# Optimization experiments

Hardware: AMD Instinct MI355X
Metric: run time of the kernel (lower is better)

Reference implementation:

```python
import jax, jax.numpy as jnp
import numpy as np

N = 100000      # nodes
E = 3200000     # edges
H = 64          # node_hidden_dim
DIN = 15        # node_input_dim
DOUT = 12       # output_dim
NT = 5          # num_edge_type
G = 256         # graphs in batch
STEPS = 6       # num_step_prop


def setup_inputs() -> dict:
    key = jax.random.key(0)
    ks = jax.random.split(key, 24)
    s = 0.1
    n = lambda k, shp: jax.random.normal(k, shp, jnp.float32) * s
    return {
        "x": jax.random.normal(ks[0], (N, DIN), jnp.float32),
        "edge_index": jax.random.randint(ks[1], (2, E), 0, N, dtype=jnp.int32),
        "edge_attr": jax.random.randint(ks[2], (E,), 0, NT, dtype=jnp.int32),
        "batch": jnp.sort(jax.random.randint(ks[3], (N,), 0, G, dtype=jnp.int32)),
        "lin0_w": n(ks[4], (DIN, H)), "lin0_b": n(ks[5], (H,)),
        "edge_embed": n(ks[6], (NT, H * H)),
        "conv_bias": n(ks[7], (H,)),
        "gru_w_ih": n(ks[8], (H, 3 * H)), "gru_w_hh": n(ks[9], (H, 3 * H)),
        "gru_b_ih": n(ks[10], (3 * H,)), "gru_b_hh": n(ks[11], (3 * H,)),
        "i_w1": n(ks[12], (2 * H, H)), "i_b1": n(ks[13], (H,)),
        "i_w2": n(ks[14], (H, DOUT)), "i_b2": n(ks[15], (DOUT,)),
        "j_w1": n(ks[16], (H, H)), "j_b1": n(ks[17], (H,)),
        "j_w2": n(ks[18], (H, DOUT)), "j_b2": n(ks[19], (DOUT,)),
    }


def reference(x, edge_index, edge_attr, batch,
              lin0_w, lin0_b, edge_embed, conv_bias,
              gru_w_ih, gru_w_hh, gru_b_ih, gru_b_hh,
              i_w1, i_b1, i_w2, i_b2, j_w1, j_b1, j_w2, j_b2):
    src, dst = edge_index[0], edge_index[1]
    W_types = edge_embed.reshape(NT, H, H)  # per edge-type [H_in, H_out]

    # in-degree for mean aggregation (PyG: isolated nodes get 0)
    deg = jax.ops.segment_sum(jnp.ones((E,), x.dtype), dst, num_segments=N)
    deg = jnp.maximum(deg, 1.0)[:, None]

    out0 = jax.nn.relu(x @ lin0_w + lin0_b)
    out = out0
    h = out0

    for _ in range(STEPS):
        # NNConv: per-edge matmul m_e = x_src[e] @ W[type_e].
        # Only NT=5 edge types exist -> precompute all 5 transforms, then gather.
        T = jnp.einsum('nh,tho->nto', out, W_types)        # [N, NT, H]
        msg = T[src, edge_attr]                            # [E, H] gather
        agg = jax.ops.segment_sum(msg, dst, num_segments=N) / deg + conv_bias
        m = jax.nn.relu(agg)

        # GRU cell (torch gate order: r, z, n)
        gx = m @ gru_w_ih + gru_b_ih
        gh = h @ gru_w_hh + gru_b_hh
        xr, xz, xn = jnp.split(gx, 3, axis=1)
        hr, hz, hn = jnp.split(gh, 3, axis=1)
        r = jax.nn.sigmoid(xr + hr)
        z = jax.nn.sigmoid(xz + hz)
        nn_ = jnp.tanh(xn + r * hn)
        h = (1.0 - z) * nn_ + z * h
        out = h

    # gated readout
    i = jax.nn.sigmoid(
        jax.nn.sigmoid(jnp.concatenate([out, out0], axis=1) @ i_w1 + i_b1) @ i_w2 + i_b2)
    j = jax.nn.sigmoid(out @ j_w1 + j_b1) @ j_w2 + j_b2
    gated = i * j                                          # [N, DOUT]
    return jax.ops.segment_sum(gated, batch, num_segments=G)  # [G, DOUT]
```

## Files before the change

kernel.cpp:

```cpp
#include <hip/hip_runtime.h>
#include <hip/hip_bf16.h>

typedef __hip_bfloat16 bf16;
using short8 = __attribute__((ext_vector_type(8))) short;
using f32x4  = __attribute__((ext_vector_type(4))) float;
using f32x2  = __attribute__((ext_vector_type(2))) float;

#define MFMA16(a,b,c) __builtin_amdgcn_mfma_f32_16x16x32_bf16((a),(b),(c),0,0,0)
#define MAXBUCK 4096
#define SB 72
#define MSTR 72
#define SRCCAP 1024
#define CHK 8192
#define BCAP 2816

__device__ __forceinline__ float b2f(bf16 v){ return __bfloat162float(v); }
__device__ __forceinline__ bf16  f2b(float v){ return __float2bfloat16(v); }
__device__ __forceinline__ float sigmf(float x){ return 1.f/(1.f+__expf(-x)); }
__device__ __forceinline__ float tanhfast(float x){
  x = fminf(fmaxf(x,-15.f),15.f);
  float e = __expf(2.f*x);
  return (e-1.f)/(e+1.f);
}
__device__ __forceinline__ short8 ld_frag(const bf16* p){
  return *reinterpret_cast<const short8*>(p);
}
__device__ __forceinline__ short f2bits(float f){
  unsigned u = __builtin_bit_cast(unsigned, f);
  unsigned r = (u + 0x7FFFu + ((u>>16)&1u)) >> 16;
  return (short)r;
}
__device__ __forceinline__ f32x2 pk_add(f32x2 a, f32x2 b){
  f32x2 d;
  asm("v_pk_add_f32 %0, %1, %2" : "=v"(d) : "v"(a), "v"(b));
  return d;
}
__device__ __forceinline__ unsigned cvtpk_bf16(float lo, float hi){
  unsigned r;
  asm("v_cvt_pk_bf16_f32 %0, %1, %2" : "=v"(r) : "v"(lo), "v"(hi));
  return r;
}

__device__ __forceinline__ f32x2 cvt8lo(unsigned w){
  f32x2 r;
  asm("v_cvt_pk_f32_fp8 %0, %1" : "=v"(r) : "v"(w));
  return r;
}
__device__ __forceinline__ f32x2 cvt8hi(unsigned w){
  return cvt8lo(w >> 16);
}
__device__ __forceinline__ unsigned short f32pair_to_fp8(float a, float b){
  unsigned r = 0;
  asm("v_cvt_pk_fp8_f32 %0, %1, %2" : "+v"(r) : "v"(a), "v"(b));
  return (unsigned short)(r & 0xffffu);
}


__global__ void k_sniff(const unsigned int* __restrict__ x, int* __restrict__ flag){
  int t = threadIdx.x;
  int good = 0;
  for (int i=t; i<4096; i+=256){
    unsigned w = x[i];
    unsigned e = (w>>23)&0xFFu;
    unsigned m = w & 0x7FFFFFFFu;
    if ((e>=100u && e<=150u) || m==0u) good++;
  }
  __shared__ int sm[256];
  sm[t]=good; __syncthreads();
  if (t==0){ int s=0; for (int k=0;k<256;k++) s+=sm[k]; *flag = (s>2048)?1:0; }
}

struct PtrPack { const void* p[17]; };

#define CAN_X     0
#define CAN_L0W   1500032
#define CAN_L0B   1500992
#define CAN_EE    1501056
#define CAN_CB    1521536
#define CAN_WIH   1521600
#define CAN_WHH   1533888
#define CAN_BIH   1546176
#define CAN_BHH   1546368
#define CAN_IW1   1546560
#define CAN_IB1   1554752
#define CAN_IW2   1554816
#define CAN_IB2   1555584
#define CAN_JW1   1555648
#define CAN_JB1   1559744
#define CAN_JW2   1559808
#define CAN_JB2   1560576
#define CAN_TOT   1560640

__global__ void k_canon(PtrPack pk, const int* __restrict__ flag, bf16* __restrict__ dst){
  static const int offs[17] = {CAN_X,CAN_L0W,CAN_L0B,CAN_EE,CAN_CB,CAN_WIH,CAN_WHH,
    CAN_BIH,CAN_BHH,CAN_IW1,CAN_IB1,CAN_IW2,CAN_IB2,CAN_JW1,CAN_JB1,CAN_JW2,CAN_JB2};
  static const int szs[17]  = {1500000,960,64,20480,64,12288,12288,192,192,8192,64,768,12,4096,64,768,12};
  int t = blockIdx.x*256+threadIdx.x;
  if (t >= CAN_TOT) return;
  int s = 0;
  #pragma unroll
  for (int k=1;k<17;k++) if (t >= offs[k]) s = k;
  int i = t - offs[s];
  float v = 0.f;
  if (i < szs[s]){
    if (*flag) v = ((const float*)pk.p[s])[i];
    else       v = b2f(((const bf16*)pk.p[s])[i]);
  }
  dst[t] = f2b(v);
}


__global__ __launch_bounds__(1024) void k_scan(const int* __restrict__ cnt, int n,
      int* __restrict__ ptr, int* __restrict__ cursor){
  __shared__ int ws[17];
  int tid = threadIdx.x, lane = tid&63, w = tid>>6;
  int run = 0;
  for (int base=0; base<n; base+=1024){
    int i = base + tid;
    int v = (i<n)? cnt[i] : 0;
    int incl = v;
    #pragma unroll
    for (int off=1; off<64; off<<=1){
      int t = __shfl_up(incl, off, 64);
      if (lane>=off) incl += t;
    }
    if (lane==63) ws[w] = incl;
    __syncthreads();
    if (tid==0){ int r=0; for (int k=0;k<16;k++){ int t=ws[k]; ws[k]=r; r+=t; } ws[16]=r; }
    __syncthreads();
    int excl = run + ws[w] + incl - v;
    if (i<n){
      ptr[i] = excl;
      if (cursor) cursor[i] = excl;
    }
    run += ws[16];
    __syncthreads();
  }
  if (tid==0) ptr[n] = run;
}

__global__ __launch_bounds__(512) void k_csort(const int* __restrict__ srcv,
      const int* __restrict__ dstv, const int* __restrict__ eav, int E_, int nb, int NC,
      unsigned int* __restrict__ bucketed, int* __restrict__ rs, int* __restrict__ bkt_cnt){
  __shared__ int lh[MAXBUCK];
  __shared__ int lofs[MAXBUCK];
  __shared__ int ws[9];
  int c = blockIdx.x, tid = threadIdx.x;
  int base = c*CHK, end = min(base+CHK, E_);
  for (int i=tid;i<nb;i+=512) lh[i]=0;
  __syncthreads();
  for (int i=base+tid; i<end; i+=512) atomicAdd(&lh[dstv[i]>>5], 1);
  __syncthreads();
  int lane=tid&63, w=tid>>6;
  int run=0;
  for (int bb=0; bb<nb; bb+=512){
    int i=bb+tid;
    int v=(i<nb)? lh[i]:0;
    int incl=v;
    #pragma unroll
    for (int off=1;off<64;off<<=1){
      int t=__shfl_up(incl,off,64);
      if (lane>=off) incl+=t;
    }
    if (lane==63) ws[w]=incl;
    __syncthreads();
    if (tid==0){ int r=0; for(int k=0;k<8;k++){int t=ws[k];ws[k]=r;r+=t;} ws[8]=r; }
    __syncthreads();
    if (i<nb) lofs[i]= run + ws[w] + incl - v;
    run += ws[8];
    __syncthreads();
  }
  for (int i=tid;i<nb;i+=512){
    rs[(size_t)i*NC + c] = base + lofs[i];
    int cntv = lh[i];
    if (cntv) atomicAdd(&bkt_cnt[i], cntv);
  }
  if (tid==0) rs[(size_t)nb*NC + c] = end;
  __syncthreads();
  for (int i=base+tid;i<end;i+=512){
    int d = dstv[i];
    int bin = d>>5;
    int pos = base + atomicAdd(&lofs[bin], 1);
    bucketed[pos] = (((unsigned)((d&31)*5 + eav[i]))<<17) | (unsigned)srcv[i];
  }
}

__global__ __launch_bounds__(256) void k_bsort2(const unsigned int* __restrict__ bucketed,
      const int* __restrict__ rs, int NC,
      const int* __restrict__ bkt_ptr, int nb, int E_,
      int* __restrict__ kptr, int* __restrict__ sorted_src,
      unsigned char* __restrict__ kperm){
  __shared__ unsigned sbuf[BCAP];
  __shared__ int rofs[1025];
  __shared__ int cnt[160], sc[160], cur[160];
  int b = blockIdx.x, tid = threadIdx.x;
  int s = bkt_ptr[b], e = bkt_ptr[b+1];
  int size = e - s;
  const int* rowA = rs + (size_t)b*NC;
  const int* rowB = rs + (size_t)(b+1)*NC;
  for (int c2=tid; c2<NC; c2+=256) rofs[c2] = rowB[c2] - rowA[c2];
  __syncthreads();
  if (tid==0){
    int acc=0;
    for (int c2=0;c2<NC;c2++){ int t=rofs[c2]; rofs[c2]=acc; acc+=t; }
    rofs[NC]=acc;
  }
  __syncthreads();
  bool staged = (size <= BCAP);
  if (staged){
    for (int c2=tid; c2<NC; c2+=256){
      int st = rowA[c2];
      int ln = rowB[c2] - st;
      int d0 = rofs[c2];
      for (int k=0;k<ln;k++) sbuf[d0+k] = bucketed[st+k];
    }
  }
  __syncthreads();
  if (tid<160) cnt[tid]=0;
  __syncthreads();
  if (staged){
    for (int i=tid;i<size;i+=256) atomicAdd(&cnt[sbuf[i]>>17], 1);
  } else {
    for (int c2=0;c2<NC;c2++){
      int st=rowA[c2], ln=rowB[c2]-st;
      for (int k=tid;k<ln;k+=256) atomicAdd(&cnt[bucketed[st+k]>>17], 1);
    }
  }
  __syncthreads();
  if (tid<160) sc[tid]=cnt[tid];
  __syncthreads();
  #pragma unroll
  for (int off=1; off<160; off<<=1){
    int v = 0;
    if (tid<160 && tid>=off) v = sc[tid-off];
    __syncthreads();
    if (tid<160) sc[tid] += v;
    __syncthreads();
  }
  if (tid<160){
    int basek = s + sc[tid] - cnt[tid];
    kptr[b*160+tid] = basek;
    cur[tid] = basek;
  }
  if (b==nb-1 && tid==0) kptr[(size_t)nb*160] = e;
  if (tid<160){
    int hbase = (tid<80)? 0 : 80;
    int me = cnt[tid];
    int r = 0;
    for (int j=0;j<80;j++){
      int jj = hbase+j;
      int cj = cnt[jj];
      r += (cj>me) || (cj==me && jj<tid);
    }
    kperm[((size_t)b*2 + (tid<80?0:1))*80 + r] = (unsigned char)(tid - hbase);
  }
  __syncthreads();
  if (staged){
    for (int i=tid;i<size;i+=256){
      unsigned p = sbuf[i];
      int pos = atomicAdd(&cur[p>>17], 1);
      sorted_src[pos] = (int)(p & 0x1FFFFu);
    }
  } else {
    for (int c2=0;c2<NC;c2++){
      int st=rowA[c2], ln=rowB[c2]-st;
      for (int k=tid;k<ln;k+=256){
        unsigned p = bucketed[st+k];
        int pos = atomicAdd(&cur[p>>17], 1);
        sorted_src[pos] = (int)(p & 0x1FFFFu);
      }
    }
  }
}

__global__ __launch_bounds__(256) void k_lin0(const bf16* __restrict__ x,
      const bf16* __restrict__ w, const bf16* __restrict__ b,
      bf16* __restrict__ out0, bf16* __restrict__ h,
      unsigned char* __restrict__ hq, int N_){
  int idx = blockIdx.x*256+threadIdx.x;
  int n = idx>>6, o = idx&63;
  if (n>=N_) return;
  float acc = b2f(b[o]);
  #pragma unroll
  for (int k=0;k<15;k++) acc += b2f(x[n*15+k]) * b2f(w[k*64+o]);
  float hv = fmaxf(acc,0.f);
  bf16 v = f2b(hv);
  out0[idx]=v; h[idx]=v;
  float hvn = __shfl_xor(hv, 1);
  if (!(o&1)) *(unsigned short*)(hq + (size_t)n*64 + o) = f32pair_to_fp8(hv, hvn);
}

__device__ __forceinline__ void d_swz(const unsigned short* src, int KS, int NC,
                                      unsigned short* dst, int nfrag, int t){
  if (t >= nfrag*64) return;
  int lane=t&63, frag=t>>6, cb=frag/KS, ks=frag%KS;
  int c = cb*16 + (lane&15);
  #pragma unroll
  for (int j=0;j<8;j++){
    int k = ks*32 + ((lane>>4)<<3) + j;
    dst[t*8+j] = (c<NC)? src[k*NC+c] : (unsigned short)0;
  }
}

__global__ __launch_bounds__(256) void k_prep(const bf16* __restrict__ ee,
      const bf16* __restrict__ wih, const bf16* __restrict__ whh,
      const bf16* __restrict__ iw1, const bf16* __restrict__ jw1,
      const bf16* __restrict__ iw2, const bf16* __restrict__ jw2,
      unsigned short* __restrict__ wall, unsigned short* __restrict__ wgru,
      unsigned short* __restrict__ wr1, unsigned short* __restrict__ wiw2s,
      unsigned short* __restrict__ wjw2s,
      const int* __restrict__ batch, int N_, int G_, int* __restrict__ gptr){
  int blk = blockIdx.x, tid = threadIdx.x;
  if (blk < 10){
    int t = blk*256+tid;
    if (t<2560){
      int lane=t&63, frag=t>>6, ct=frag/10, ks=frag%10;
      int c = ct*16 + (lane&15);
      #pragma unroll
      for (int j=0;j<8;j++){
        int k = ks*32 + ((lane>>4)<<3) + j;
        int tt = k>>6, kc = k&63;
        wall[t*8+j] = ((const unsigned short*)ee)[tt*4096 + kc*64 + c];
      }
    }
  } else if (blk < 16){
    d_swz((const unsigned short*)wih, 2, 192, wgru, 24, (blk-10)*256+tid);
  } else if (blk < 22){
    d_swz((const unsigned short*)whh, 2, 192, wgru+12288, 24, (blk-16)*256+tid);
  } else if (blk < 26){
    d_swz((const unsigned short*)iw1, 4, 64, wr1, 16, (blk-22)*256+tid);
  } else if (blk < 28){
    d_swz((const unsigned short*)jw1, 2, 64, wr1+8192, 8, (blk-26)*256+tid);
  } else if (blk == 28){
    d_swz((const unsigned short*)iw2, 2, 12, wiw2s, 2, tid);
  } else if (blk == 29){
    d_swz((const unsigned short*)jw2, 2, 12, wjw2s, 2, tid);
  } else {
    int g = (blk-30)*256+tid;
    if (g <= G_){
      int lo=0, hi=N_;
      while (lo<hi){ int mid=(lo+hi)>>1; if (batch[mid] < g) lo=mid+1; else hi=mid; }
      gptr[g]=lo;
    }
  }
}

__global__ __launch_bounds__(256,8) void k_step(const bf16* __restrict__ hin,
      bf16* __restrict__ hout,
      const unsigned char* __restrict__ hqin, unsigned char* __restrict__ hqout,
      const int* __restrict__ sorted_src, const int* __restrict__ kptr,
      const unsigned char* __restrict__ kperm,
      const unsigned short* __restrict__ wall, const unsigned short* __restrict__ wgru,
      const bf16* __restrict__ conv_bias, const bf16* __restrict__ bih,
      const bf16* __restrict__ bhh, int N_){
  __shared__ unsigned short Sb[80*SB];
  __shared__ int kp[81];
  __shared__ unsigned char pm[80];
  __shared__ char ubuf[SRCCAP*4 + 32];
  int* srcL = (int*)ubuf;
  unsigned short* m_s = (unsigned short*)ubuf;
  int tid=threadIdx.x, lane=tid&63, w=tid>>6;
  int b=blockIdx.x;
  if (tid<81) kp[tid]=kptr[(size_t)b*80+tid];
  if (tid<80) pm[tid]=kperm[(size_t)b*80+tid];
  __syncthreads();
  int s0g = kp[0];
  int elen = kp[80]-s0g;
  int cap = (elen<=SRCCAP)? elen : 0;
  for (int i=tid;i<cap;i+=256) srcL[i]=sorted_src[s0g+i]<<6;
  __syncthreads();
  int g=lane>>3, c=lane&7;
  const unsigned char* hp8 = hqin + (c<<3);
  const int sent = N_<<6;

  auto run_phase1 = [&](auto GET){
    #pragma unroll 1
    for (int jo=0;jo<5;jo++){
      int pbase = jo*16 + w*4;
      int p  = pm[pbase + (g&3)];
      int p0 = pm[pbase];
      int st = kp[p]-s0g, len = kp[p+1]-kp[p];
      int maxLen = kp[p0+1]-kp[p0];
      int sub = g>>2;
      f32x2 a01={0.f,0.f}, a23={0.f,0.f}, a45={0.f,0.f}, a67={0.f,0.f};
      for (int base=0; base<maxLen; base+=8){
        uint2 hv[4];
        #pragma unroll
        for (int u=0;u<4;u++){
          int idx = base + sub*4 + u;
          int s = GET(st+idx);
          s = (idx < len)? s : sent;
          hv[u] = *(const uint2*)(hp8 + (size_t)s);
        }
        #pragma unroll
        for (int u=0;u<4;u++){
          a01 = pk_add(a01, cvt8lo(hv[u].x));
          a23 = pk_add(a23, cvt8hi(hv[u].x));
          a45 = pk_add(a45, cvt8lo(hv[u].y));
          a67 = pk_add(a67, cvt8hi(hv[u].y));
        }
      }
      float a[8] = {a01.x,a01.y,a23.x,a23.y,a45.x,a45.y,a67.x,a67.y};
      #pragma unroll
      for (int j=0;j<8;j++) a[j] += __shfl_xor(a[j], 32);
      if (g<4){
        uint4 v;
        v.x = cvtpk_bf16(a[0],a[1]);
        v.y = cvtpk_bf16(a[2],a[3]);
        v.z = cvtpk_bf16(a[4],a[5]);
        v.w = cvtpk_bf16(a[6],a[7]);
        *reinterpret_cast<uint4*>(&Sb[(size_t)p*SB + c*8]) = v;
      }
    }
  };
  if (cap) run_phase1([&](int rel){ return srcL[rel]; });
  else     run_phase1([&](int rel){ return sorted_src[s0g+rel]<<6; });
  __syncthreads();

  int q=lane>>4, mr=lane&15;
  {
    int ct = w;
    f32x4 acc={0.f,0.f,0.f,0.f};
    #pragma unroll
    for (int ks=0;ks<10;ks++){
      int k0 = ks*32 + q*8;
      int tt = k0>>6, ch = k0&63;
      short8 af = *reinterpret_cast<const short8*>(&Sb[(size_t)(mr*5+tt)*SB + ch]);
      short8 bfrag = *(const short8*)(wall + (size_t)((ct*10+ks)*64+lane)*8);
      acc = MFMA16(af, bfrag, acc);
    }
    int col = ct*16+mr;
    float bi = b2f(conv_bias[col]);
    #pragma unroll
    for (int r=0;r<4;r++){
      int nl = q*4+r;
      int deg = kp[nl*5+5]-kp[nl*5];
      float dv = 1.f/fmaxf((float)deg,1.f);
      m_s[nl*MSTR+col] = (unsigned short)f2bits(fmaxf(acc[r]*dv+bi,0.f));
    }
  }
  __syncthreads();

  {
    int cc = w;
    int na = b*16+mr; if (na>N_-1) na=N_-1;
    short8 am0 = *(const short8*)(&m_s[mr*MSTR + q*8]);
    short8 am1 = *(const short8*)(&m_s[mr*MSTR + 32 + q*8]);
    short8 ah0 = ld_frag(hin + (size_t)na*64 + q*8);
    short8 ah1 = ld_frag(hin + (size_t)na*64 + 32 + q*8);
    const short8* Bw = reinterpret_cast<const short8*>(wgru);
    f32x4 xr={0.f,0.f,0.f,0.f}, xz=xr, xn=xr, hr=xr, hz=xr, hn=xr;
    xr = MFMA16(am0, Bw[((cc  )*2+0)*64+lane], xr);
    xr = MFMA16(am1, Bw[((cc  )*2+1)*64+lane], xr);
    xz = MFMA16(am0, Bw[((cc+4)*2+0)*64+lane], xz);
    xz = MFMA16(am1, Bw[((cc+4)*2+1)*64+lane], xz);
    xn = MFMA16(am0, Bw[((cc+8)*2+0)*64+lane], xn);
    xn = MFMA16(am1, Bw[((cc+8)*2+1)*64+lane], xn);
    hr = MFMA16(ah0, Bw[(24+(cc  )*2+0)*64+lane], hr);
    hr = MFMA16(ah1, Bw[(24+(cc  )*2+1)*64+lane], hr);
    hz = MFMA16(ah0, Bw[(24+(cc+4)*2+0)*64+lane], hz);
    hz = MFMA16(ah1, Bw[(24+(cc+4)*2+1)*64+lane], hz);
    hn = MFMA16(ah0, Bw[(24+(cc+8)*2+0)*64+lane], hn);
    hn = MFMA16(ah1, Bw[(24+(cc+8)*2+1)*64+lane], hn);
    int col = cc*16+mr;
    float bxr=b2f(bih[col]), bxz=b2f(bih[col+64]), bxn=b2f(bih[col+128]);
    float bhr=b2f(bhh[col]), bhz=b2f(bhh[col+64]), bhn=b2f(bhh[col+128]);
    #pragma unroll
    for (int r=0;r<4;r++){
      int row = q*4+r;
      int n = b*16+row;
      int nc = (n<N_)? n : N_-1;
      float rg = sigmf(xr[r]+bxr + hr[r]+bhr);
      float zg = sigmf(xz[r]+bxz + hz[r]+bhz);
      float ng = tanhfast(xn[r]+bxn + rg*(hn[r]+bhn));
      float ho = b2f(hin[(size_t)nc*64+col]);
      float hv = (1.f-zg)*ng + zg*ho;
      float hvn = __shfl_xor(hv, 1);
      if (n < N_){
        hout[(size_t)n*64+col] = f2b(hv);
        if (!(mr&1))
          *(unsigned short*)(hqout + (size_t)n*64 + col) = f32pair_to_fp8(hv, hvn);
      }
    }
  }
}

__global__ __launch_bounds__(256) void k_read(const bf16* __restrict__ h, const bf16* __restrict__ out0,
      const unsigned short* __restrict__ W, const bf16* __restrict__ ib1, const bf16* __restrict__ jb1,
      const unsigned short* __restrict__ iw2swz, const unsigned short* __restrict__ jw2swz,
      const bf16* __restrict__ ib2, const bf16* __restrict__ jb2,
      float* __restrict__ gated, int N_){
  __shared__ unsigned short lds[12288];
  __shared__ unsigned short sbuf[64*72];
  __shared__ unsigned short tbuf[64*72];
  { const int* s=(const int*)W; int* d=(int*)lds;
    for (int i=threadIdx.x;i<6144;i+=256) d[i]=s[i]; }
  __syncthreads();
  int tid=threadIdx.x, lane=tid&63, w=tid>>6, q=lane>>4;
  int nb = blockIdx.x*64 + w*16;
  int ar = nb + (lane&15); if (ar>N_-1) ar=N_-1;
  short8 ah0 = ld_frag(h + (size_t)ar*64 + q*8),    ah1 = ld_frag(h + (size_t)ar*64 + 32 + q*8);
  short8 ao0 = ld_frag(out0 + (size_t)ar*64 + q*8), ao1 = ld_frag(out0 + (size_t)ar*64 + 32 + q*8);
  const short8* Bi = reinterpret_cast<const short8*>(lds);
  const short8* Bj = reinterpret_cast<const short8*>(lds + 8192);
  int colb = lane&15;
  for (int cb=0; cb<4; cb++){
    f32x4 ai = {0.f,0.f,0.f,0.f};
    ai = MFMA16(ah0, Bi[(cb*4+0)*64+lane], ai);
    ai = MFMA16(ah1, Bi[(cb*4+1)*64+lane], ai);
    ai = MFMA16(ao0, Bi[(cb*4+2)*64+lane], ai);
    ai = MFMA16(ao1, Bi[(cb*4+3)*64+lane], ai);
    f32x4 aj = {0.f,0.f,0.f,0.f};
    aj = MFMA16(ah0, Bj[(cb*2+0)*64+lane], aj);
    aj = MFMA16(ah1, Bj[(cb*2+1)*64+lane], aj);
    int col = cb*16 + colb;
    float bi=b2f(ib1[col]), bj=b2f(jb1[col]);
    #pragma unroll
    for (int r=0;r<4;r++){
      int lrow = w*16 + q*4 + r;
      sbuf[lrow*72+col] = (unsigned short)f2bits(sigmf(ai[r]+bi));
      tbuf[lrow*72+col] = (unsigned short)f2bits(sigmf(aj[r]+bj));
    }
  }
  __syncthreads();
  int mr = lane&15;
  short8 as0 = *(const short8*)(&sbuf[(w*16+mr)*72 + q*8]);
  short8 as1 = *(const short8*)(&sbuf[(w*16+mr)*72 + 32 + q*8]);
  short8 at0 = *(const short8*)(&tbuf[(w*16+mr)*72 + q*8]);
  short8 at1 = *(const short8*)(&tbuf[(w*16+mr)*72 + 32 + q*8]);
  const short8* Bi2 = reinterpret_cast<const short8*>(iw2swz);
  const short8* Bj2 = reinterpret_cast<const short8*>(jw2swz);
  f32x4 ai = {0.f,0.f,0.f,0.f};
  ai = MFMA16(as0, Bi2[lane], ai);
  ai = MFMA16(as1, Bi2[64+lane], ai);
  f32x4 aj = {0.f,0.f,0.f,0.f};
  aj = MFMA16(at0, Bj2[lane], aj);
  aj = MFMA16(at1, Bj2[64+lane], aj);
  int col = lane&15;
  if (col<12){
    float bi=b2f(ib2[col]), bj=b2f(jb2[col]);
    #pragma unroll
    for (int r=0;r<4;r++){
      int row = nb + q*4 + r;
      if (row < N_) gated[(size_t)row*12+col] = sigmf(ai[r]+bi)*(aj[r]+bj);
    }
  }
}

__global__ __launch_bounds__(256) void k_graphsum(const float* __restrict__ gated,
      const int* __restrict__ gptr, const int* __restrict__ flag, void* __restrict__ outp){
  int g = blockIdx.x;
  int s = gptr[g], e = gptr[g+1];
  int tid = threadIdx.x;
  int c = tid & 15, rg = tid >> 4;
  float acc = 0.f;
  if (c < 12)
    for (int row = s + rg; row < e; row += 16) acc += gated[(size_t)row*12 + c];
  __shared__ float sm[256];
  sm[tid] = acc;
  __syncthreads();
  if (rg == 0 && c < 12){
    float t = 0.f;
    for (int k=0;k<16;k++) t += sm[k*16 + c];
    if (*flag) ((float*)outp)[g*12 + c] = t;
    else       ((bf16*) outp)[g*12 + c] = f2b(t);
  }
}


extern "C" void kernel_launch(void* const* d_in, const int* in_sizes, int n_in,
                              void* d_out, int out_size, void* d_ws, size_t ws_size,
                              hipStream_t stream){
  const int*  ei    = (const int*) d_in[1];
  const int*  ea    = (const int*) d_in[2];
  const int*  batch = (const int*) d_in[3];

  const int N_ = in_sizes[3];
  const int E_ = in_sizes[2];
  const int G_ = out_size / 12;
  const int nb  = (N_ + 31) >> 5;
  const int nbs = (N_ + 15) >> 4;
  const int NC  = (E_ + CHK - 1) / CHK;

  char* ws = (char*)d_ws;
  size_t off = 0;
  auto alloc = [&](size_t bytes)->size_t{
    size_t o = off; off += (bytes + 255) & ~(size_t)255; return o;
  };

  size_t oOut0   = alloc((size_t)N_*64*2);
  size_t oH0     = alloc((size_t)(N_+1)*64*2);
  size_t oH1     = alloc((size_t)(N_+1)*64*2);
  size_t oHq0    = alloc((size_t)(N_+1)*64);
  size_t oHq1    = alloc((size_t)(N_+1)*64);
  size_t oGated  = alloc((size_t)N_*12*4);
  size_t oBEdges = alloc((size_t)E_*4);
  size_t oSorted = alloc((size_t)E_*4 + 256);
  size_t oRS     = alloc((size_t)(nb+1)*NC*4);
  size_t oKptr   = alloc(((size_t)nb*160+2)*4);
  size_t oKperm  = alloc((size_t)nb*160);
  size_t oCanon  = alloc((size_t)CAN_TOT*2);
  size_t oCnt    = alloc((size_t)nb*4);
  size_t oBPtr   = alloc((size_t)(nb+1)*4);
  size_t oGptr   = alloc((size_t)(G_+1)*4);
  size_t oFlag   = alloc(256);
  size_t oWall   = alloc((size_t)20480*2);
  size_t oWgru   = alloc((size_t)24576*2);
  size_t oWr1    = alloc((size_t)12288*2);
  size_t oWiw2   = alloc((size_t)1024*2);
  size_t oWjw2   = alloc((size_t)1024*2);

  bf16*  out0    = (bf16*)(ws + oOut0);
  bf16*  h0      = (bf16*)(ws + oH0);
  bf16*  h1      = (bf16*)(ws + oH1);
  unsigned char* hq0 = (unsigned char*)(ws + oHq0);
  unsigned char* hq1 = (unsigned char*)(ws + oHq1);
  float* gated   = (float*)(ws + oGated);
  unsigned int* bucketed = (unsigned int*)(ws + oBEdges);
  int*   sorted_src = (int*)(ws + oSorted);
  int*   rs      = (int*)(ws + oRS);
  int*   kptr    = (int*)(ws + oKptr);
  unsigned char* kperm = (unsigned char*)(ws + oKperm);
  bf16*  can     = (bf16*)(ws + oCanon);
  int*   bkt_cnt = (int*)(ws + oCnt);
  int*   bkt_ptr = (int*)(ws + oBPtr);
  int*   gptr    = (int*)(ws + oGptr);
  int*   flag    = (int*)(ws + oFlag);
  unsigned short* wall  = (unsigned short*)(ws + oWall);
  unsigned short* wgru  = (unsigned short*)(ws + oWgru);
  unsigned short* wr1   = (unsigned short*)(ws + oWr1);
  unsigned short* wiw2s = (unsigned short*)(ws + oWiw2);
  unsigned short* wjw2s = (unsigned short*)(ws + oWjw2);

  const bf16* xC    = can + CAN_X;
  const bf16* l0wC  = can + CAN_L0W;
  const bf16* l0bC  = can + CAN_L0B;
  const bf16* eeC   = can + CAN_EE;
  const bf16* cbC   = can + CAN_CB;
  const bf16* wihC  = can + CAN_WIH;
  const bf16* whhC  = can + CAN_WHH;
  const bf16* bihC  = can + CAN_BIH;
  const bf16* bhhC  = can + CAN_BHH;
  const bf16* iw1C  = can + CAN_IW1;
  const bf16* ib1C  = can + CAN_IB1;
  const bf16* iw2C  = can + CAN_IW2;
  const bf16* ib2C  = can + CAN_IB2;
  const bf16* jw1C  = can + CAN_JW1;
  const bf16* jb1C  = can + CAN_JB1;
  const bf16* jw2C  = can + CAN_JW2;
  const bf16* jb2C  = can + CAN_JB2;

  PtrPack pk;
  pk.p[0]=d_in[0];  pk.p[1]=d_in[4];  pk.p[2]=d_in[5];  pk.p[3]=d_in[6];
  pk.p[4]=d_in[7];  pk.p[5]=d_in[8];  pk.p[6]=d_in[9];  pk.p[7]=d_in[10];
  pk.p[8]=d_in[11]; pk.p[9]=d_in[12]; pk.p[10]=d_in[13]; pk.p[11]=d_in[14];
  pk.p[12]=d_in[15]; pk.p[13]=d_in[16]; pk.p[14]=d_in[17]; pk.p[15]=d_in[18];
  pk.p[16]=d_in[19];

  const int gNw  = (N_+63)/64;

  k_sniff<<<1, 256, 0, stream>>>((const unsigned int*)d_in[0], flag);
  k_canon<<<(CAN_TOT+255)/256, 256, 0, stream>>>(pk, flag, can);
  hipMemsetAsync(ws + oCnt, 0, (size_t)nb*4, stream);
  hipMemsetAsync(ws + oH0 + (size_t)N_*128, 0, 128, stream);
  hipMemsetAsync(ws + oH1 + (size_t)N_*128, 0, 128, stream);
  hipMemsetAsync(ws + oHq0 + (size_t)N_*64, 0, 64, stream);
  hipMemsetAsync(ws + oHq1 + (size_t)N_*64, 0, 64, stream);
  k_csort<<<NC, 512, 0, stream>>>(ei, ei + E_, ea, E_, nb, NC, bucketed, rs, bkt_cnt);
  k_scan<<<1, 1024, 0, stream>>>(bkt_cnt, nb, bkt_ptr, nullptr);
  k_bsort2<<<nb, 256, 0, stream>>>(bucketed, rs, NC, bkt_ptr, nb, E_, kptr, sorted_src, kperm);
  k_lin0<<<(N_*64+255)/256, 256, 0, stream>>>(xC, l0wC, l0bC, out0, h0, hq0, N_);
  k_prep<<<32, 256, 0, stream>>>(eeC, wihC, whhC, iw1C, jw1C, iw2C, jw2C,
                                 wall, wgru, wr1, wiw2s, wjw2s, batch, N_, G_, gptr);

  bf16* hb[2] = {h0, h1};
  unsigned char* hqb[2] = {hq0, hq1};
  for (int step = 0; step < 6; ++step){
    k_step<<<nbs, 256, 0, stream>>>(hb[step&1], hb[(step+1)&1],
                                    hqb[step&1], hqb[(step+1)&1],
                                    sorted_src, kptr, kperm,
                                    wall, wgru, cbC, bihC, bhhC, N_);
  }
  bf16* hfin = hb[0];

  k_read<<<gNw, 256, 0, stream>>>(hfin, out0, wr1, ib1C, jb1C, wiw2s, wjw2s,
                                  ib2C, jb2C, gated, N_);
  k_graphsum<<<G_, 256, 0, stream>>>(gated, gptr, flag, d_out);
}
```

Baseline: 669.0 us.

## Fold memsets into sniff kernel, enlarge sort chunks, parallelize bucket staging

```diff
diff --git a/kernel.cpp b/kernel.cpp
--- a/kernel.cpp
+++ b/kernel.cpp
@@ -11,7 +11,8 @@
 #define SB 72
 #define MSTR 72
 #define SRCCAP 1024
-#define CHK 8192
+#define CHK 32768
+#define MAXNC 128
 #define BCAP 2816
 
 __device__ __forceinline__ float b2f(bf16 v){ return __bfloat162float(v); }
@@ -55,9 +56,20 @@
   return (unsigned short)(r & 0xffffu);
 }
 
-
-__global__ void k_sniff(const unsigned int* __restrict__ x, int* __restrict__ flag){
+__global__ void k_sniff(const unsigned int* __restrict__ x, int* __restrict__ flag,
+      int* __restrict__ bkt_cnt, int nb,
+      int* __restrict__ s0, int* __restrict__ s1,
+      int* __restrict__ s2, int* __restrict__ s3){
   int t = threadIdx.x;
+  if (blockIdx.x == 1){
+    for (int i=t;i<nb;i+=256) bkt_cnt[i]=0;
+    return;
+  }
+  if (blockIdx.x == 2){
+    if (t<32){ s0[t]=0; s1[t]=0; }
+    if (t<16){ s2[t]=0; s3[t]=0; }
+    return;
+  }
   int good = 0;
   for (int i=t; i<4096; i+=256){
     unsigned w = x[i];
@@ -139,21 +151,21 @@
   if (tid==0) ptr[n] = run;
 }
 
-__global__ __launch_bounds__(512) void k_csort(const int* __restrict__ srcv,
+__global__ __launch_bounds__(1024) void k_csort(const int* __restrict__ srcv,
       const int* __restrict__ dstv, const int* __restrict__ eav, int E_, int nb, int NC,
       unsigned int* __restrict__ bucketed, int* __restrict__ rs, int* __restrict__ bkt_cnt){
   __shared__ int lh[MAXBUCK];
   __shared__ int lofs[MAXBUCK];
-  __shared__ int ws[9];
+  __shared__ int ws[17];
   int c = blockIdx.x, tid = threadIdx.x;
   int base = c*CHK, end = min(base+CHK, E_);
-  for (int i=tid;i<nb;i+=512) lh[i]=0;
-  __syncthreads();
-  for (int i=base+tid; i<end; i+=512) atomicAdd(&lh[dstv[i]>>5], 1);
+  for (int i=tid;i<nb;i+=1024) lh[i]=0;
+  __syncthreads();
+  for (int i=base+tid; i<end; i+=1024) atomicAdd(&lh[dstv[i]>>5], 1);
   __syncthreads();
   int lane=tid&63, w=tid>>6;
   int run=0;
-  for (int bb=0; bb<nb; bb+=512){
+  for (int bb=0; bb<nb; bb+=1024){
     int i=bb+tid;
     int v=(i<nb)? lh[i]:0;
     int incl=v;
@@ -164,20 +176,20 @@
     }
     if (lane==63) ws[w]=incl;
     __syncthreads();
-    if (tid==0){ int r=0; for(int k=0;k<8;k++){int t=ws[k];ws[k]=r;r+=t;} ws[8]=r; }
+    if (tid==0){ int r=0; for(int k=0;k<16;k++){int t=ws[k];ws[k]=r;r+=t;} ws[16]=r; }
     __syncthreads();
     if (i<nb) lofs[i]= run + ws[w] + incl - v;
-    run += ws[8];
-    __syncthreads();
-  }
-  for (int i=tid;i<nb;i+=512){
+    run += ws[16];
+    __syncthreads();
+  }
+  for (int i=tid;i<nb;i+=1024){
     rs[(size_t)i*NC + c] = base + lofs[i];
     int cntv = lh[i];
     if (cntv) atomicAdd(&bkt_cnt[i], cntv);
   }
   if (tid==0) rs[(size_t)nb*NC + c] = end;
   __syncthreads();
-  for (int i=base+tid;i<end;i+=512){
+  for (int i=base+tid;i<end;i+=1024){
     int d = dstv[i];
     int bin = d>>5;
     int pos = base + atomicAdd(&lofs[bin], 1);
@@ -191,28 +203,46 @@
       int* __restrict__ kptr, int* __restrict__ sorted_src,
       unsigned char* __restrict__ kperm){
   __shared__ unsigned sbuf[BCAP];
-  __shared__ int rofs[1025];
+  __shared__ int rofs[MAXNC+1];
+  __shared__ int rstart[MAXNC];
+  __shared__ int scan2[2][MAXNC];
   __shared__ int cnt[160], sc[160], cur[160];
   int b = blockIdx.x, tid = threadIdx.x;
   int s = bkt_ptr[b], e = bkt_ptr[b+1];
   int size = e - s;
   const int* rowA = rs + (size_t)b*NC;
   const int* rowB = rs + (size_t)(b+1)*NC;
-  for (int c2=tid; c2<NC; c2+=256) rofs[c2] = rowB[c2] - rowA[c2];
-  __syncthreads();
-  if (tid==0){
-    int acc=0;
-    for (int c2=0;c2<NC;c2++){ int t=rofs[c2]; rofs[c2]=acc; acc+=t; }
-    rofs[NC]=acc;
-  }
-  __syncthreads();
-  bool staged = (size <= BCAP);
+  bool fits = (NC <= MAXNC);
+  if (fits){
+    int v = 0;
+    if (tid < NC){
+      int a = rowA[tid];
+      rstart[tid] = a;
+      v = rowB[tid] - a;
+    }
+    if (tid < MAXNC) scan2[0][tid] = v;
+    __syncthreads();
+    int pp = 0;
+    #pragma unroll
+    for (int off=1; off<MAXNC; off<<=1){
+      if (tid < MAXNC){
+        int nv = scan2[pp][tid];
+        if (tid>=off) nv += scan2[pp][tid-off];
+        scan2[pp^1][tid] = nv;
+      }
+      __syncthreads();
+      pp ^= 1;
+    }
+    if (tid==0) rofs[0]=0;
+    if (tid < NC) rofs[tid+1] = scan2[pp][tid];
+    __syncthreads();
+  }
+  bool staged = fits && (size <= BCAP);
   if (staged){
-    for (int c2=tid; c2<NC; c2+=256){
-      int st = rowA[c2];
-      int ln = rowB[c2] - st;
-      int d0 = rofs[c2];
-      for (int k=0;k<ln;k++) sbuf[d0+k] = bucketed[st+k];
+    for (int i=tid; i<size; i+=256){
+      int lo=0, hi=NC-1;
+      while (lo<hi){ int mid=(lo+hi+1)>>1; if (rofs[mid]<=i) lo=mid; else hi=mid-1; }
+      sbuf[i] = bucketed[rstart[lo] + (i - rofs[lo])];
     }
   }
   __syncthreads();
@@ -659,14 +689,14 @@
 
   const int gNw  = (N_+63)/64;
 
-  k_sniff<<<1, 256, 0, stream>>>((const unsigned int*)d_in[0], flag);
+  k_sniff<<<3, 256, 0, stream>>>((const unsigned int*)d_in[0], flag,
+                                 bkt_cnt, nb,
+                                 (int*)(ws + oH0 + (size_t)N_*128),
+                                 (int*)(ws + oH1 + (size_t)N_*128),
+                                 (int*)(ws + oHq0 + (size_t)N_*64),
+                                 (int*)(ws + oHq1 + (size_t)N_*64));
   k_canon<<<(CAN_TOT+255)/256, 256, 0, stream>>>(pk, flag, can);
-  hipMemsetAsync(ws + oCnt, 0, (size_t)nb*4, stream);
-  hipMemsetAsync(ws + oH0 + (size_t)N_*128, 0, 128, stream);
-  hipMemsetAsync(ws + oH1 + (size_t)N_*128, 0, 128, stream);
-  hipMemsetAsync(ws + oHq0 + (size_t)N_*64, 0, 64, stream);
-  hipMemsetAsync(ws + oHq1 + (size_t)N_*64, 0, 64, stream);
-  k_csort<<<NC, 512, 0, stream>>>(ei, ei + E_, ea, E_, nb, NC, bucketed, rs, bkt_cnt);
+  k_csort<<<NC, 1024, 0, stream>>>(ei, ei + E_, ea, E_, nb, NC, bucketed, rs, bkt_cnt);
   k_scan<<<1, 1024, 0, stream>>>(bkt_cnt, nb, bkt_ptr, nullptr);
   k_bsort2<<<nb, 256, 0, stream>>>(bucketed, rs, NC, bkt_ptr, nb, E_, kptr, sorted_src, kperm);
   k_lin0<<<(N_*64+255)/256, 256, 0, stream>>>(xC, l0wC, l0bC, out0, h0, hq0, N_);
```

After: 680.3 us. No clear change (+1.7%).
